# Kernel optimization log

Hardware: AMD Instinct MI355X
Metric: run time of the kernel (lower is better)

The kernel has to match this reference:

```python
import jax, jax.numpy as jnp
import numpy as np

N = 8192
D = 128
NUM_INSTANCES = 8  # samples per class (balanced PK batch)
ALPHA = 50.0
BASE = 1.0


def setup_inputs() -> dict:
    key = jax.random.key(0)
    k1, = jax.random.split(key, 1)
    x = jax.random.normal(k1, (N, D), dtype=jnp.float32)
    # L2-normalize so pairwise dists ~ sqrt(2) and exp(alpha*(1-d)) stays finite in fp32
    inputs = x / jnp.linalg.norm(x, axis=1, keepdims=True)
    targets = (jnp.arange(N) // NUM_INSTANCES).astype(jnp.int64)
    return {"inputs": inputs, "targets": targets}


def _euclidean_dist(x):
    sq = jnp.sum(x * x, axis=1)  # [n]
    d2 = sq[:, None] + sq[None, :] - 2.0 * (x @ x.T)  # [n, n]
    return jnp.sqrt(jnp.clip(d2, 1e-12, None))


def reference(inputs, targets):
    n = inputs.shape[0]
    dist = _euclidean_dist(inputs)                      # [n, n]
    same = targets[:, None] == targets[None, :]         # [n, n] bool
    eye = jnp.eye(n, dtype=bool)
    pos_mask = same & ~eye                              # positives, excluding self
    neg_mask = ~same                                    # negatives

    e = jnp.exp(ALPHA * (BASE - dist))                  # [n, n]
    pos_logit = jnp.sum(jnp.where(pos_mask, e, 0.0), axis=1)        # [n]
    neg_logit = jnp.sum(jnp.where(neg_mask, e, 0.0), axis=1) * 0.5  # [n]
    loss = jnp.mean(-jnp.log(pos_logit / (pos_logit + neg_logit)))

    pos_d = jnp.sum(jnp.where(pos_mask, dist, 0.0)) / jnp.sum(pos_mask)
    neg_d = jnp.sum(jnp.where(neg_mask, dist, 0.0)) / jnp.sum(neg_mask)
    prec = jnp.float32(1.0)  # err is always 0 in the original code
    return (loss, prec, pos_d, neg_d)
```

## Files before the change

### kernel.cpp

```cpp
#include <hip/hip_runtime.h>

#define NN 8192
#define DD 128
#define C2 72.13475204444817f
#define LN2 0.6931471805599453f
#define NTILE 64

typedef __attribute__((ext_vector_type(8))) __bf16 bf16x8;
typedef __attribute__((ext_vector_type(4))) float f32x4;

#if __has_builtin(__builtin_amdgcn_exp2f)
#define EXP2F(x) __builtin_amdgcn_exp2f(x)
#else
#define EXP2F(x) exp2f(x)
#endif
#if __has_builtin(__builtin_amdgcn_sqrtf)
#define SQRTF(x) __builtin_amdgcn_sqrtf(x)
#else
#define SQRTF(x) sqrtf(x)
#endif
#if __has_builtin(__builtin_amdgcn_logf)
#define LOG2F(x) __builtin_amdgcn_logf(x)
#else
#define LOG2F(x) log2f(x)
#endif

__device__ __forceinline__ unsigned short f2bf(float f) {
  unsigned u = __float_as_uint(f);
  u += 0x7FFFu + ((u >> 16) & 1u);
  return (unsigned short)(u >> 16);
}

__device__ __forceinline__ void gload_lds16(const void* g, void* l) {
  __builtin_amdgcn_global_load_lds(
      (const __attribute__((address_space(1))) void*)g,
      (__attribute__((address_space(3))) void*)l, 16, 0, 0);
}

__global__ __launch_bounds__(512) void prep_pos_kernel(
    const float* __restrict__ x, unsigned short* __restrict__ xbf,
    float* __restrict__ sq, float* __restrict__ pos_e,
    float* __restrict__ pos_d, float* __restrict__ accs,
    unsigned* __restrict__ cnt) {
  int w = threadIdx.x >> 6;
  int lane = threadIdx.x & 63;
  int i = blockIdx.x * 8 + w;

  __shared__ float xs[8][128];
  __shared__ float sqs[8];

  const float* xr = x + (size_t)i * DD;
  float a = xr[lane], b = xr[lane + 64];
  xs[w][lane] = a;
  xs[w][lane + 64] = b;

  float s = __fmaf_rn(a, a, b * b);
#pragma unroll
  for (int m = 32; m; m >>= 1) s += __shfl_xor(s, m, 64);
  if (lane == 0) {
    sq[i] = s;
    sqs[w] = s;
  }
  unsigned short* o = xbf + (size_t)i * DD;
  int t1 = lane >> 3, e1 = lane & 7;
  o[((t1 ^ w) << 3) + e1] = f2bf(a);
  o[64 + ((t1 ^ w) << 3) + e1] = f2bf(b);
  if (blockIdx.x == 0) {
    if (threadIdx.x == 0) {
      accs[0] = 0.f;
      accs[1] = 0.f;
      accs[2] = 0.f;
    }
    if (threadIdx.x == 1) cnt[0] = 0u;
  }

  __syncthreads();
  float sqi = sqs[w];
  float pe = 0.f, pd = 0.f;
  for (int j = 0; j < 8; ++j) {
    if (j == w) continue;
    float dot = __fmaf_rn(a, xs[j][lane], b * xs[j][lane + 64]);
#pragma unroll
    for (int m = 32; m; m >>= 1) dot += __shfl_xor(dot, m, 64);
    float d2 = fmaxf(__fmaf_rn(-2.f, dot, sqi + sqs[j]), 1e-12f);
    float dist = SQRTF(d2);
    pe += EXP2F(__fmaf_rn(dist, -C2, C2));
    pd += dist;
  }
  if (lane == 0) {
    pos_e[i] = pe;
    pos_d[i] = pd;
  }
}

__global__ __launch_bounds__(256, 1) void tile_kernel(
    const unsigned short* __restrict__ xbf, const float* __restrict__ sq,
    float* __restrict__ part, float* __restrict__ dpart) {
  int lane = threadIdx.x & 63;
  int wave = threadIdx.x >> 6;
  int q = lane >> 4, c = lane & 15;
  int p = blockIdx.x >> 4;
  int s = blockIdx.x & 15;
  int rA = p, rB = 63 - p;
  int nA = 64 - p;
  int k0 = (65 * s) >> 4, k1 = (65 * (s + 1)) >> 4;

  __shared__ char panelA[65536];
  __shared__ char panelB[65536];
  __shared__ float rowsumW[4][64];
  __shared__ float colsumW[4][64];
  __shared__ float partd[4];

  int goff = wave * 1024 + lane * 16;
  {
    const char* gA0 = (const char*)xbf + (size_t)rA * 32768;
    const char* gA1 = (const char*)xbf + (size_t)rB * 32768;
    char* lA = panelA + wave * 1024;
#pragma unroll
    for (int t = 0; t < 8; ++t) {
      gload_lds16(gA0 + t * 4096 + goff, lA + t * 4096);
      gload_lds16(gA1 + t * 4096 + goff, lA + 32768 + t * 4096);
    }
    int tc0 = (k0 < nA) ? (rA + k0) : (rB + (k0 - nA));
    const char* gB = (const char*)xbf + (size_t)tc0 * 32768;
    char* lB = panelB + wave * 1024;
#pragma unroll
    for (int t = 0; t < 8; ++t) gload_lds16(gB + t * 4096 + goff, lB + t * 4096);
  }

  float dacc = 0.f;
  int swz = (c & 7) << 4;

  __syncthreads();

  for (int k = k0; k < k1; ++k) {
    int cur = (k - k0) & 1;
    if (k + 1 < k1) {
      int kn = k + 1;
      int tcn = (kn < nA) ? (rA + kn) : (rB + (kn - nA));
      const char* gB = (const char*)xbf + (size_t)tcn * 32768;
      char* lB = panelB + (cur ^ 1) * 32768 + wave * 1024;
#pragma unroll
      for (int t = 0; t < 8; ++t)
        gload_lds16(gB + t * 4096 + goff, lB + t * 4096);
    }
    int inB = (k >= nA) ? 1 : 0;
    int row = inB ? rB : rA;
    int tc = inB ? (rB + (k - nA)) : (rA + k);
    bool diag = (row == tc);
    int I0 = row * 128 + (wave >> 1) * 64;
    int J0 = tc * 128 + (wave & 1) * 64;

    float sqi[16];
#pragma unroll
    for (int rb = 0; rb < 4; ++rb)
#pragma unroll
      for (int r = 0; r < 4; ++r)
        sqi[rb * 4 + r] = sq[I0 + rb * 16 + q * 4 + r];
    float sqj[4];
#pragma unroll
    for (int cb = 0; cb < 4; ++cb) sqj[cb] = sq[J0 + cb * 16 + c];

    f32x4 acc[4][4];
#pragma unroll
    for (int rb = 0; rb < 4; ++rb)
#pragma unroll
      for (int cb = 0; cb < 4; ++cb)
        acc[rb][cb] = (f32x4){0.f, 0.f, 0.f, 0.f};

    {
      const char* pa = panelA + inB * 32768 + (wave >> 1) * 16384 + c * 256;
      const char* pb = panelB + cur * 32768 + (wave & 1) * 16384 + c * 256;
#pragma unroll
      for (int ks = 0; ks < 4; ++ks) {
        int koff = (ks * 64 + q * 16) ^ swz;
        bf16x8 ar[4], br[4];
#pragma unroll
        for (int rb = 0; rb < 4; ++rb)
          ar[rb] = *(const bf16x8*)(pa + rb * 4096 + koff);
#pragma unroll
        for (int cb = 0; cb < 4; ++cb)
          br[cb] = *(const bf16x8*)(pb + cb * 4096 + koff);
#pragma unroll
        for (int rb = 0; rb < 4; ++rb)
#pragma unroll
          for (int cb = 0; cb < 4; ++cb)
            acc[rb][cb] = __builtin_amdgcn_mfma_f32_16x16x32_bf16(
                ar[rb], br[cb], acc[rb][cb], 0, 0, 0);
      }
    }

    float tote[16];
#pragma unroll
    for (int kk = 0; kk < 16; ++kk) tote[kk] = 0.f;
    float pcol[4] = {0.f, 0.f, 0.f, 0.f};
    float totd = 0.f;

#pragma unroll
    for (int rb = 0; rb < 4; ++rb) {
#pragma unroll
      for (int cb = 0; cb < 4; ++cb) {
        bool diagTile = (I0 + rb * 16) == (J0 + cb * 16);
#pragma unroll
        for (int r = 0; r < 4; ++r) {
          float d2 = fmaxf(
              __fmaf_rn(-2.f, acc[rb][cb][r], sqi[rb * 4 + r] + sqj[cb]),
              1e-12f);
          float dist = SQRTF(d2);
          float ex = EXP2F(__fmaf_rn(dist, -C2, C2));
          if (diagTile && (q * 4 + r) == c) {
            ex = 0.f;
            dist = 0.f;
          }
          tote[rb * 4 + r] += ex;
          pcol[cb] += ex;
          totd += dist;
        }
      }
    }
    dacc += diag ? totd : 2.f * totd;

#pragma unroll
    for (int kk = 0; kk < 16; ++kk) {
      float v = tote[kk];
      v += __shfl_xor(v, 1, 64);
      v += __shfl_xor(v, 2, 64);
      v += __shfl_xor(v, 4, 64);
      v += __shfl_xor(v, 8, 64);
      tote[kk] = v;
    }
    if (c == 0) {
#pragma unroll
      for (int rb = 0; rb < 4; ++rb)
#pragma unroll
        for (int r = 0; r < 4; ++r)
          rowsumW[wave][rb * 16 + q * 4 + r] = tote[rb * 4 + r];
    }
#pragma unroll
    for (int cb = 0; cb < 4; ++cb) {
      float cs = pcol[cb];
      cs += __shfl_xor(cs, 16, 64);
      cs += __shfl_xor(cs, 32, 64);
      if (q == 0) colsumW[wave][cb * 16 + c] = cs;
    }

    __syncthreads();

    size_t rslot = ((size_t)row * NTILE + tc) * 128;
    size_t cslot = ((size_t)tc * NTILE + row) * 128;
    int t = threadIdx.x;
    if (t < 128) {
      part[rslot + t] =
          rowsumW[(t >> 6) * 2][t & 63] + rowsumW[(t >> 6) * 2 + 1][t & 63];
    } else if (!diag) {
      int t2 = t - 128;
      part[cslot + t2] =
          colsumW[t2 >> 6][t2 & 63] + colsumW[(t2 >> 6) + 2][t2 & 63];
    }
    __syncthreads();
  }

#pragma unroll
  for (int m = 32; m; m >>= 1) dacc += __shfl_xor(dacc, m, 64);
  if (lane == 0) partd[wave] = dacc;
  __syncthreads();
  if (threadIdx.x == 0)
    dpart[blockIdx.x] = partd[0] + partd[1] + partd[2] + partd[3];
}

__global__ __launch_bounds__(128) void fin_kernel(
    const float* __restrict__ part, const float* __restrict__ dpart,
    const float* __restrict__ pos_e, const float* __restrict__ pos_d,
    float* accs, unsigned* cnt, float* __restrict__ out) {
  int a = blockIdx.x, c = threadIdx.x;
  const float* pa = part + (size_t)a * NTILE * 128 + c;
  float tot = 0.f;
#pragma unroll
  for (int t = 0; t < 64; ++t) tot += pa[(size_t)t * 128];
  int i = a * 128 + c;
  float p = pos_e[i];
  float denom = __fmaf_rn(0.5f, tot - p, p);
  float lsum = LOG2F(denom) - LOG2F(p);
  float pdsum = pos_d[i];
  float ds = (c < 8) ? dpart[a * 8 + c] : 0.f;

  __shared__ float s1[128], s2[128], s3[128];
  s1[c] = lsum;
  s2[c] = pdsum;
  s3[c] = ds;
  __syncthreads();
  for (int w = 64; w; w >>= 1) {
    if (c < w) {
      s1[c] += s1[c + w];
      s2[c] += s2[c + w];
      s3[c] += s3[c + w];
    }
    __syncthreads();
  }
  if (c == 0) {
    atomicAdd(&accs[0], s1[0]);
    atomicAdd(&accs[1], s2[0]);
    atomicAdd(&accs[2], s3[0]);
    __threadfence();
    unsigned old = atomicAdd(cnt, 1u);
    if (old == 63u) {
      float L = atomicAdd(&accs[0], 0.f);
      float PD = atomicAdd(&accs[1], 0.f);
      float DS = atomicAdd(&accs[2], 0.f);
      out[0] = L * LN2 / (float)NN;
      out[1] = 1.0f;
      out[2] = PD / (float)(NN * 7);
      out[3] = (DS - PD) / ((float)NN * 8184.f);
    }
  }
}

extern "C" void kernel_launch(void* const* d_in, const int* in_sizes, int n_in,
                              void* d_out, int out_size, void* d_ws,
                              size_t ws_size, hipStream_t stream) {
  const float* x = (const float*)d_in[0];
  float* out = (float*)d_out;
  char* ws = (char*)d_ws;

  unsigned short* xbf = (unsigned short*)ws;
  float* sq = (float*)(ws + (size_t)NN * DD * 2);
  float* pos_e = sq + NN;
  float* pos_d = pos_e + NN;
  float* part = pos_d + NN;
  float* dpart = part + (size_t)NTILE * NTILE * 128;
  float* accs = dpart + 512;
  unsigned* cnt = (unsigned*)(accs + 3);

  prep_pos_kernel<<<NN / 8, 512, 0, stream>>>(x, xbf, sq, pos_e, pos_d, accs,
                                              cnt);
  tile_kernel<<<512, 256, 0, stream>>>(xbf, sq, part, dpart);
  fin_kernel<<<64, 128, 0, stream>>>(part, dpart, pos_e, pos_d, accs, cnt,
                                     out);
}
```

Measured before the change: 109.7 us.

## Walk upper-triangle tiles linearly with A fragments in registers and 8 waves

The row-pair panel scheme is replaced by a linear walk over the 2080 upper-triangle tiles, with each block taking a contiguous range. The A-row fragments are loaded straight from global memory into registers and reloaded only when the tile row changes, which frees the 64KB A panel in LDS. Blocks now run 8 waves of 32x64 sub-tiles at up to 3 blocks per CU, and the row and column partial sums are double-buffered by iteration so the trailing barrier can be dropped. The aim is higher occupancy and less LDS traffic. The cost is more global loads for A fragments and more register pressure.

After: 105.3 us. -4.0%, faster.

```diff
diff --git a/kernel.cpp b/kernel.cpp
--- a/kernel.cpp
+++ b/kernel.cpp
@@ -5,6 +5,8 @@
 #define C2 72.13475204444817f
 #define LN2 0.6931471805599453f
 #define NTILE 64
+#define NTRI 2080
+#define NBLK 512
 
 typedef __attribute__((ext_vector_type(8))) __bf16 bf16x8;
 typedef __attribute__((ext_vector_type(4))) float f32x4;
@@ -93,67 +95,69 @@
   }
 }
 
-__global__ __launch_bounds__(256, 1) void tile_kernel(
+__global__ __launch_bounds__(512, 3) void tile_kernel(
     const unsigned short* __restrict__ xbf, const float* __restrict__ sq,
     float* __restrict__ part, float* __restrict__ dpart) {
   int lane = threadIdx.x & 63;
   int wave = threadIdx.x >> 6;
   int q = lane >> 4, c = lane & 15;
-  int p = blockIdx.x >> 4;
-  int s = blockIdx.x & 15;
-  int rA = p, rB = 63 - p;
-  int nA = 64 - p;
-  int k0 = (65 * s) >> 4, k1 = (65 * (s + 1)) >> 4;
-
-  __shared__ char panelA[65536];
+  int rq = wave >> 1, ch = wave & 1;
+
+  int k0 = (65 * blockIdx.x) >> 4, k1 = (65 * (blockIdx.x + 1)) >> 4;
+  int tr = (int)((129.0f - SQRTF(16641.0f - 8.0f * (float)k0)) * 0.5f);
+  while (tr > 0 && tr * (129 - tr) / 2 > k0) --tr;
+  while ((tr + 1) * (128 - tr) / 2 <= k0) ++tr;
+  int tc = tr + (k0 - tr * (129 - tr) / 2);
+
   __shared__ char panelB[65536];
-  __shared__ float rowsumW[4][64];
-  __shared__ float colsumW[4][64];
-  __shared__ float partd[4];
-
-  int goff = wave * 1024 + lane * 16;
+  __shared__ float rowsumW[2][2][128];
+  __shared__ float colsumW[2][4][128];
+  __shared__ float partd[8];
+
+  int goffB = wave * 4096 + lane * 16;
   {
-    const char* gA0 = (const char*)xbf + (size_t)rA * 32768;
-    const char* gA1 = (const char*)xbf + (size_t)rB * 32768;
-    char* lA = panelA + wave * 1024;
-#pragma unroll
-    for (int t = 0; t < 8; ++t) {
-      gload_lds16(gA0 + t * 4096 + goff, lA + t * 4096);
-      gload_lds16(gA1 + t * 4096 + goff, lA + 32768 + t * 4096);
-    }
-    int tc0 = (k0 < nA) ? (rA + k0) : (rB + (k0 - nA));
-    const char* gB = (const char*)xbf + (size_t)tc0 * 32768;
-    char* lB = panelB + wave * 1024;
-#pragma unroll
-    for (int t = 0; t < 8; ++t) gload_lds16(gB + t * 4096 + goff, lB + t * 4096);
-  }
-
+    const char* gB = (const char*)xbf + (size_t)tc * 32768;
+    char* lB = panelB + wave * 4096;
+#pragma unroll
+    for (int t = 0; t < 4; ++t) gload_lds16(gB + t * 1024 + goffB, lB + t * 1024);
+  }
+
+  bf16x8 ar[2][4];
+  int atr = -1;
   float dacc = 0.f;
-  int swz = (c & 7) << 4;
+  int swz8 = (c & 7);
 
   __syncthreads();
 
   for (int k = k0; k < k1; ++k) {
     int cur = (k - k0) & 1;
     if (k + 1 < k1) {
-      int kn = k + 1;
-      int tcn = (kn < nA) ? (rA + kn) : (rB + (kn - nA));
+      int tcn = (tc + 1 < 64) ? tc + 1 : tr + 1;
       const char* gB = (const char*)xbf + (size_t)tcn * 32768;
-      char* lB = panelB + (cur ^ 1) * 32768 + wave * 1024;
-#pragma unroll
-      for (int t = 0; t < 8; ++t)
-        gload_lds16(gB + t * 4096 + goff, lB + t * 4096);
-    }
-    int inB = (k >= nA) ? 1 : 0;
-    int row = inB ? rB : rA;
-    int tc = inB ? (rB + (k - nA)) : (rA + k);
-    bool diag = (row == tc);
-    int I0 = row * 128 + (wave >> 1) * 64;
-    int J0 = tc * 128 + (wave & 1) * 64;
-
-    float sqi[16];
-#pragma unroll
-    for (int rb = 0; rb < 4; ++rb)
+      char* lB = panelB + (cur ^ 1) * 32768 + wave * 4096;
+#pragma unroll
+      for (int t = 0; t < 4; ++t)
+        gload_lds16(gB + t * 1024 + goffB, lB + t * 1024);
+    }
+
+    int I0 = tr * 128 + rq * 32;
+    int J0 = tc * 128 + ch * 64;
+    bool diag = (tr == tc);
+
+    if (atr != tr) {
+      atr = tr;
+#pragma unroll
+      for (int rb = 0; rb < 2; ++rb) {
+        const unsigned short* rp = xbf + (size_t)(I0 + rb * 16 + c) * DD;
+#pragma unroll
+        for (int ks = 0; ks < 4; ++ks)
+          ar[rb][ks] = *(const bf16x8*)(rp + (((ks * 4 + q) ^ swz8) << 3));
+      }
+    }
+
+    float sqi[8];
+#pragma unroll
+    for (int rb = 0; rb < 2; ++rb)
 #pragma unroll
       for (int r = 0; r < 4; ++r)
         sqi[rb * 4 + r] = sq[I0 + rb * 16 + q * 4 + r];
@@ -161,43 +165,39 @@
 #pragma unroll
     for (int cb = 0; cb < 4; ++cb) sqj[cb] = sq[J0 + cb * 16 + c];
 
-    f32x4 acc[4][4];
-#pragma unroll
-    for (int rb = 0; rb < 4; ++rb)
+    f32x4 acc[2][4];
+#pragma unroll
+    for (int rb = 0; rb < 2; ++rb)
 #pragma unroll
       for (int cb = 0; cb < 4; ++cb)
         acc[rb][cb] = (f32x4){0.f, 0.f, 0.f, 0.f};
 
     {
-      const char* pa = panelA + inB * 32768 + (wave >> 1) * 16384 + c * 256;
-      const char* pb = panelB + cur * 32768 + (wave & 1) * 16384 + c * 256;
+      const char* pb = panelB + cur * 32768 + ch * 16384 + c * 256;
 #pragma unroll
       for (int ks = 0; ks < 4; ++ks) {
-        int koff = (ks * 64 + q * 16) ^ swz;
-        bf16x8 ar[4], br[4];
-#pragma unroll
-        for (int rb = 0; rb < 4; ++rb)
-          ar[rb] = *(const bf16x8*)(pa + rb * 4096 + koff);
+        int koff = (ks * 64 + q * 16) ^ (swz8 << 4);
+        bf16x8 br[4];
 #pragma unroll
         for (int cb = 0; cb < 4; ++cb)
           br[cb] = *(const bf16x8*)(pb + cb * 4096 + koff);
 #pragma unroll
-        for (int rb = 0; rb < 4; ++rb)
+        for (int rb = 0; rb < 2; ++rb)
 #pragma unroll
           for (int cb = 0; cb < 4; ++cb)
             acc[rb][cb] = __builtin_amdgcn_mfma_f32_16x16x32_bf16(
-                ar[rb], br[cb], acc[rb][cb], 0, 0, 0);
+                ar[rb][ks], br[cb], acc[rb][cb], 0, 0, 0);
       }
     }
 
-    float tote[16];
-#pragma unroll
-    for (int kk = 0; kk < 16; ++kk) tote[kk] = 0.f;
+    float tote[8];
+#pragma unroll
+    for (int kk = 0; kk < 8; ++kk) tote[kk] = 0.f;
     float pcol[4] = {0.f, 0.f, 0.f, 0.f};
     float totd = 0.f;
 
 #pragma unroll
-    for (int rb = 0; rb < 4; ++rb) {
+    for (int rb = 0; rb < 2; ++rb) {
 #pragma unroll
       for (int cb = 0; cb < 4; ++cb) {
         bool diagTile = (I0 + rb * 16) == (J0 + cb * 16);
@@ -221,7 +221,7 @@
     dacc += diag ? totd : 2.f * totd;
 
 #pragma unroll
-    for (int kk = 0; kk < 16; ++kk) {
+    for (int kk = 0; kk < 8; ++kk) {
       float v = tote[kk];
       v += __shfl_xor(v, 1, 64);
       v += __shfl_xor(v, 2, 64);
@@ -231,41 +231,49 @@
     }
     if (c == 0) {
 #pragma unroll
-      for (int rb = 0; rb < 4; ++rb)
+      for (int rb = 0; rb < 2; ++rb)
 #pragma unroll
         for (int r = 0; r < 4; ++r)
-          rowsumW[wave][rb * 16 + q * 4 + r] = tote[rb * 4 + r];
+          rowsumW[cur][ch][rq * 32 + rb * 16 + q * 4 + r] = tote[rb * 4 + r];
     }
 #pragma unroll
     for (int cb = 0; cb < 4; ++cb) {
       float cs = pcol[cb];
       cs += __shfl_xor(cs, 16, 64);
       cs += __shfl_xor(cs, 32, 64);
-      if (q == 0) colsumW[wave][cb * 16 + c] = cs;
+      if (q == 0) colsumW[cur][rq][ch * 64 + cb * 16 + c] = cs;
     }
 
     __syncthreads();
 
-    size_t rslot = ((size_t)row * NTILE + tc) * 128;
-    size_t cslot = ((size_t)tc * NTILE + row) * 128;
+    size_t rslot = ((size_t)tr * NTILE + tc) * 128;
+    size_t cslot = ((size_t)tc * NTILE + tr) * 128;
     int t = threadIdx.x;
     if (t < 128) {
-      part[rslot + t] =
-          rowsumW[(t >> 6) * 2][t & 63] + rowsumW[(t >> 6) * 2 + 1][t & 63];
-    } else if (!diag) {
+      part[rslot + t] = rowsumW[cur][0][t] + rowsumW[cur][1][t];
+    } else if (t < 256 && !diag) {
       int t2 = t - 128;
-      part[cslot + t2] =
-          colsumW[t2 >> 6][t2 & 63] + colsumW[(t2 >> 6) + 2][t2 & 63];
-    }
-    __syncthreads();
+      part[cslot + t2] = colsumW[cur][0][t2] + colsumW[cur][1][t2] +
+                         colsumW[cur][2][t2] + colsumW[cur][3][t2];
+    }
+    if (tc + 1 < 64) {
+      ++tc;
+    } else {
+      ++tr;
+      tc = tr;
+    }
   }
 
 #pragma unroll
   for (int m = 32; m; m >>= 1) dacc += __shfl_xor(dacc, m, 64);
   if (lane == 0) partd[wave] = dacc;
   __syncthreads();
-  if (threadIdx.x == 0)
-    dpart[blockIdx.x] = partd[0] + partd[1] + partd[2] + partd[3];
+  if (threadIdx.x == 0) {
+    float sacc = 0.f;
+#pragma unroll
+    for (int w2 = 0; w2 < 8; ++w2) sacc += partd[w2];
+    dpart[blockIdx.x] = sacc;
+  }
 }
 
 __global__ __launch_bounds__(128) void fin_kernel(
@@ -328,12 +336,12 @@
   float* pos_d = pos_e + NN;
   float* part = pos_d + NN;
   float* dpart = part + (size_t)NTILE * NTILE * 128;
-  float* accs = dpart + 512;
+  float* accs = dpart + NBLK;
   unsigned* cnt = (unsigned*)(accs + 3);
 
   prep_pos_kernel<<<NN / 8, 512, 0, stream>>>(x, xbf, sq, pos_e, pos_d, accs,
                                               cnt);
-  tile_kernel<<<512, 256, 0, stream>>>(xbf, sq, part, dpart);
+  tile_kernel<<<NBLK, 512, 0, stream>>>(xbf, sq, part, dpart);
   fin_kernel<<<64, 128, 0, stream>>>(part, dpart, pos_e, pos_d, accs, cnt,
                                      out);
 }
```
